# Optimization experiments

Measured on AMD Instinct MI355X. Metric: run time of the kernel, lower is better.

## Reference

```python
import jax, jax.numpy as jnp
import numpy as np

D_MODEL = 1024
N_HEADS = 16
D_HEAD = D_MODEL // N_HEADS


def setup_inputs() -> dict:
    key = jax.random.key(0)
    ks = jax.random.split(key, 5)
    B, T = 2, 2048
    x = jax.random.normal(ks[0], (B, T, D_MODEL), dtype=jnp.float32)
    s = 1.0 / np.sqrt(D_MODEL)
    W_qkv = jax.random.normal(ks[1], (D_MODEL, 3 * D_MODEL), dtype=jnp.float32) * s
    b_qkv = jnp.zeros((3 * D_MODEL,), dtype=jnp.float32)
    W_proj = jax.random.normal(ks[2], (D_MODEL, D_MODEL), dtype=jnp.float32) * s
    b_proj = jnp.zeros((D_MODEL,), dtype=jnp.float32)
    return {"x": x, "W_qkv": W_qkv, "b_qkv": b_qkv, "W_proj": W_proj, "b_proj": b_proj}


def reference(x, W_qkv, b_qkv, W_proj, b_proj):
    B, T, C = x.shape
    qkv = x @ W_qkv + b_qkv                      # [B,T,3C]
    q, k, v = jnp.split(qkv, 3, axis=-1)
    # [B,T,C] -> [B,H,T,Dh]
    def to_heads(t):
        return t.reshape(B, T, N_HEADS, D_HEAD).transpose(0, 2, 1, 3)
    q, k, v = to_heads(q), to_heads(k), to_heads(v)
    scale = 1.0 / np.sqrt(D_HEAD).astype(np.float32)
    scores = jnp.einsum('bhqd,bhkd->bhqk', q, k) * scale  # [B,H,T,T]
    causal = jnp.tril(jnp.ones((T, T), dtype=bool))
    scores = jnp.where(causal, scores, -jnp.inf)
    attn = jax.nn.softmax(scores, axis=-1)
    out = jnp.einsum('bhqk,bhkd->bhqd', attn, v)          # [B,H,T,Dh]
    out = out.transpose(0, 2, 1, 3).reshape(B, T, C)
    return out @ W_proj + b_proj
```

## Files before the change

### kernel.cpp

```cpp
#include <hip/hip_runtime.h>
#include <hip/hip_bf16.h>
#include <cstdint>


using u16 = unsigned short;
using u32 = unsigned int;

typedef __bf16 bf16x8 __attribute__((ext_vector_type(8)));
typedef float f32x4 __attribute__((ext_vector_type(4)));

#define AS1 __attribute__((address_space(1)))
#define AS3 __attribute__((address_space(3)))

__device__ __forceinline__ u16 f2bf(float f) {
  u32 u = __float_as_uint(f);
  u += 0x7fffu + ((u >> 16) & 1u);
  return (u16)(u >> 16);
}
__device__ __forceinline__ u32 pack2bf(float a, float b) {
  u32 ua = __float_as_uint(a) + 0x8000u;
  u32 ub = __float_as_uint(b) + 0x8000u;
  return (ua >> 16) | (ub & 0xffff0000u);
}

__global__ __launch_bounds__(256) void prep(const float* __restrict__ x,
                                            u16* __restrict__ xb,
                                            const float* __restrict__ W0,
                                            u16* __restrict__ T0,
                                            const float* __restrict__ W1,
                                            u16* __restrict__ T1) {
  const int bx = blockIdx.x;
  const int tid = threadIdx.x;
  if (bx < 4096) {
    const int i = bx * 256 + tid;
    float4 v = ((const float4*)x)[i];
    ushort4 o;
    o.x = f2bf(v.x); o.y = f2bf(v.y); o.z = f2bf(v.z); o.w = f2bf(v.w);
    ((ushort4*)xb)[i] = o;
    return;
  }
  __shared__ float t[32][33];
  const int idx = bx - 4096;
  const int bxx = idx & 127, by = idx >> 7;
  const float* W; u16* Wt; int N, n0;
  if (bxx < 96) { W = W0; Wt = T0; N = 3072; n0 = bxx * 32; }
  else          { W = W1; Wt = T1; N = 1024; n0 = (bxx - 96) * 32; }
  const int k0 = by * 32;
  const int tx = tid & 31, ty = tid >> 5;
#pragma unroll
  for (int i = 0; i < 4; ++i)
    t[ty + i * 8][tx] = W[(size_t)(k0 + ty + i * 8) * N + n0 + tx];
  __syncthreads();
#pragma unroll
  for (int i = 0; i < 4; ++i)
    Wt[(size_t)(n0 + ty + i * 8) * 1024 + k0 + tx] = f2bf(t[tx][ty + i * 8]);
}

#define MFMA16 __builtin_amdgcn_mfma_f32_16x16x32_bf16

__global__ __launch_bounds__(512, 2) void gemm_qkv(const u16* __restrict__ A,
                                                   const u16* __restrict__ Bt,
                                                   const float* __restrict__ bias,
                                                   u16* __restrict__ qb,
                                                   u16* __restrict__ KF,
                                                   u16* __restrict__ VF,
                                                   float sc_val) {
  constexpr int NT = 16;
  constexpr int BUFO = 7 * 4096;
  __shared__ __align__(16) u16 sm[2 * BUFO];

  const int tid  = threadIdx.x;
  const int lane = tid & 63;
  const int w    = tid >> 6;
  const int quad = lane >> 4;
  const int l15  = lane & 15;

  const int bid = blockIdx.x;
  const int xcd = bid & 7, c = bid >> 3;
  const int mt = (xcd >> 1) * 4 + (c & 3);
  const int nt = (xcd & 1) * 8 + (c >> 2);
  const int bm = mt * 256, bn = nt * 192;

  const int wr = (w >> 2) * 128;
  const int wc = (w & 3) * 48;

  const int srow = tid >> 3;
  const int scol = (((tid & 7) ^ ((tid >> 3) & 7)) << 3);

#define STAGEA(ch, ktile, bufo)                                                 \
  __builtin_amdgcn_global_load_lds(                                             \
      (AS1 const void*)(A + (size_t)(bm + (ch) * 64 + srow) * 1024 +            \
                        ((ktile) << 6) + scol),                                 \
      (AS3 void*)(sm + (bufo) + (ch) * 4096 + tid * 8), 16, 0, 0)
#define STAGEB(ch, ktile, bufo)                                                 \
  __builtin_amdgcn_global_load_lds(                                             \
      (AS1 const void*)(Bt + (size_t)(bn + (ch) * 64 + srow) * 1024 +           \
                        ((ktile) << 6) + scol),                                 \
      (AS3 void*)(sm + (bufo) + (4 + (ch)) * 4096 + tid * 8), 16, 0, 0)

  const int ca = (w >> 2) * 2;
  int abase_lo[4], abase_hi[4], bbase[3];
#pragma unroll
  for (int mi = 0; mi < 4; ++mi) {
    abase_lo[mi] = (ca + 0) * 4096 + (mi * 16 + l15) * 64;
    abase_hi[mi] = (ca + 1) * 4096 + (mi * 16 + l15) * 64;
  }
#pragma unroll
  for (int ni = 0; ni < 3; ++ni) {
    const int rb = wc + ni * 16 + l15;
    bbase[ni] = (4 + (rb >> 6)) * 4096 + (rb & 63) * 64;
  }
  const int sw0 = ((quad ^ (l15 & 7)) << 3);
  const int sw1 = sw0 ^ 32;

  STAGEA(0, 0, 0); STAGEA(1, 0, 0); STAGEA(2, 0, 0); STAGEA(3, 0, 0);
  STAGEB(0, 0, 0); STAGEB(1, 0, 0); STAGEB(2, 0, 0);
  STAGEB(0, 1, BUFO); STAGEB(1, 1, BUFO);
  STAGEB(2, 1, BUFO); STAGEA(0, 1, BUFO); STAGEA(1, 1, BUFO);
  asm volatile("s_waitcnt vmcnt(5)" ::: "memory");
  __builtin_amdgcn_s_barrier();

  f32x4 acc[8][3] = {};
  bf16x8 alo[4][2], ahi[4][2], b[3][2];

#pragma unroll 2
  for (int j = 0; j < NT; ++j) {
    const int bo  = (j & 1) * BUFO;
    const int nbo = bo ^ BUFO;
    const u16* smb = sm + bo;

#pragma unroll
    for (int mi = 0; mi < 4; ++mi) {
      alo[mi][0] = *(const bf16x8*)(smb + abase_lo[mi] + sw0);
      alo[mi][1] = *(const bf16x8*)(smb + abase_lo[mi] + sw1);
    }
#pragma unroll
    for (int ni = 0; ni < 2; ++ni) {
      b[ni][0] = *(const bf16x8*)(smb + bbase[ni] + sw0);
      b[ni][1] = *(const bf16x8*)(smb + bbase[ni] + sw1);
    }
    if (j + 1 < NT) { STAGEA(2, j + 1, nbo); STAGEA(3, j + 1, nbo); }
    __builtin_amdgcn_s_barrier();
    asm volatile("s_waitcnt lgkmcnt(0)" ::: "memory");
    __builtin_amdgcn_s_setprio(1);
#pragma unroll
    for (int mi = 0; mi < 4; ++mi)
#pragma unroll
      for (int ni = 0; ni < 2; ++ni) {
        acc[mi][ni] = MFMA16(alo[mi][0], b[ni][0], acc[mi][ni], 0, 0, 0);
        acc[mi][ni] = MFMA16(alo[mi][1], b[ni][1], acc[mi][ni], 0, 0, 0);
      }
    __builtin_amdgcn_s_setprio(0);
    __builtin_amdgcn_s_barrier();

#pragma unroll
    for (int mi = 0; mi < 4; ++mi) {
      ahi[mi][0] = *(const bf16x8*)(smb + abase_hi[mi] + sw0);
      ahi[mi][1] = *(const bf16x8*)(smb + abase_hi[mi] + sw1);
    }
    b[2][0] = *(const bf16x8*)(smb + bbase[2] + sw0);
    b[2][1] = *(const bf16x8*)(smb + bbase[2] + sw1);
    if (j + 2 < NT) { STAGEB(0, j + 2, bo); STAGEB(1, j + 2, bo); }
    __builtin_amdgcn_s_barrier();
    asm volatile("s_waitcnt lgkmcnt(0)" ::: "memory");
    __builtin_amdgcn_s_setprio(1);
#pragma unroll
    for (int mi = 0; mi < 4; ++mi) {
      acc[mi][2] = MFMA16(alo[mi][0], b[2][0], acc[mi][2], 0, 0, 0);
      acc[mi][2] = MFMA16(alo[mi][1], b[2][1], acc[mi][2], 0, 0, 0);
      acc[4 + mi][0] = MFMA16(ahi[mi][0], b[0][0], acc[4 + mi][0], 0, 0, 0);
      acc[4 + mi][0] = MFMA16(ahi[mi][1], b[0][1], acc[4 + mi][0], 0, 0, 0);
    }
    __builtin_amdgcn_s_setprio(0);
    __builtin_amdgcn_s_barrier();

    if (j + 2 < NT) { STAGEB(2, j + 2, bo); STAGEA(0, j + 2, bo); STAGEA(1, j + 2, bo); }
    __builtin_amdgcn_s_barrier();
    __builtin_amdgcn_s_setprio(1);
#pragma unroll
    for (int mi = 0; mi < 4; ++mi)
#pragma unroll
      for (int ni = 1; ni < 3; ++ni) {
        acc[4 + mi][ni] = MFMA16(ahi[mi][0], b[ni][0], acc[4 + mi][ni], 0, 0, 0);
        acc[4 + mi][ni] = MFMA16(ahi[mi][1], b[ni][1], acc[4 + mi][ni], 0, 0, 0);
      }
    __builtin_amdgcn_s_setprio(0);
    if (j + 2 < NT)
      asm volatile("s_waitcnt vmcnt(5)" ::: "memory");
    else
      asm volatile("s_waitcnt vmcnt(0)" ::: "memory");
    __builtin_amdgcn_s_barrier();
  }
#undef STAGEA
#undef STAGEB

  const int crow0 = bm + wr + (quad << 2);
  const int ccol0 = bn + wc + l15;
#pragma unroll
  for (int ni = 0; ni < 3; ++ni) {
    const int n = ccol0 + ni * 16;
    const float bv = bias[n];
    if (n < 1024) {
#pragma unroll
      for (int mi = 0; mi < 8; ++mi) {
        const int m0 = crow0 + mi * 16;
#pragma unroll
        for (int r = 0; r < 4; ++r)
          qb[(size_t)(m0 + r) * 1024 + n] = f2bf((acc[mi][ni][r] + bv) * sc_val);
      }
    } else if (n < 2048) {
      const int hk = (n - 1024) >> 6;
      const int d  = (n - 1024) & 63;
      const int hh = d >> 5, qd = (d >> 3) & 3, jj = d & 7;
#pragma unroll
      for (int mi = 0; mi < 8; ++mi) {
#pragma unroll
        for (int r = 0; r < 4; ++r) {
          const int t  = crow0 + mi * 16 + r;
          const int bb = t >> 11, tt = t & 2047;
          const int kt = tt >> 6, mm = (tt >> 4) & 3, l = tt & 15;
          KF[((size_t)((bb * 16 + hk) * 32 + kt) * 8 + mm * 2 + hh) * 512 +
             (qd * 16 + l) * 8 + jj] = f2bf(acc[mi][ni][r] + bv);
        }
      }
    } else {
      const int hv = (n - 2048) >> 6;
      const int d  = (n - 2048) & 63;
      const int di = d >> 4, l = d & 15;
#pragma unroll
      for (int mi = 0; mi < 8; ++mi) {
#pragma unroll
        for (int r = 0; r < 4; ++r) {
          const int t  = crow0 + mi * 16 + r;
          const int bb = t >> 11, tt = t & 2047;
          const int kt = tt >> 6, to = tt & 63;
          const int mq = to >> 4, qd2 = (to >> 2) & 3, rr = to & 3;
          const int hh = mq >> 1, jj = (mq & 1) * 4 + rr;
          VF[((size_t)((bb * 16 + hv) * 32 + kt) * 8 + hh * 4 + di) * 512 +
             (qd2 * 16 + l) * 8 + jj] = f2bf(acc[mi][ni][r] + bv);
        }
      }
    }
  }
}

__global__ __launch_bounds__(256) void gemm_proj(const u16* __restrict__ A,
                                                 const u16* __restrict__ Bt,
                                                 const float* __restrict__ bias,
                                                 float* __restrict__ C) {
  constexpr int BM = 128, BN = 64, BK = 32;
  constexpr int K = 1024, N = 1024;
  __shared__ __align__(16) u16 lA[BM * BK];
  __shared__ __align__(16) u16 lB[BN * BK];
  const int tid  = threadIdx.x;
  const int lane = tid & 63;
  const int wave = tid >> 6;
  const int bm = blockIdx.x * BM;
  const int bn = blockIdx.y * BN;
  const int wr = wave * 32;

  f32x4 acc[2][4] = {};

  const int f0 = (wave << 10) + (lane << 4);
  const int f1 = f0 + 4096;
  const int ar0 = f0 >> 6, ac0 = (f0 & 63) >> 1;
  const int ar1 = f1 >> 6, ac1 = (f1 & 63) >> 1;

  const int arow = wr + (lane & 15);
  const int brow = (lane & 15);
  const int kk   = (lane >> 4) << 3;

  for (int k0 = 0; k0 < K; k0 += BK) {
    __builtin_amdgcn_global_load_lds((AS1 const void*)(A + (size_t)(bm + ar0) * K + k0 + ac0),
                                     (AS3 void*)(lA + (wave << 9)), 16, 0, 0);
    __builtin_amdgcn_global_load_lds((AS1 const void*)(A + (size_t)(bm + ar1) * K + k0 + ac1),
                                     (AS3 void*)(lA + ((wave + 4) << 9)), 16, 0, 0);
    __builtin_amdgcn_global_load_lds((AS1 const void*)(Bt + (size_t)(bn + ar0) * K + k0 + ac0),
                                     (AS3 void*)(lB + (wave << 9)), 16, 0, 0);
    __syncthreads();

    bf16x8 af[2], bfr[4];
#pragma unroll
    for (int mi = 0; mi < 2; ++mi)
      af[mi] = *(const bf16x8*)&lA[(arow + mi * 16) * BK + kk];
#pragma unroll
    for (int ni = 0; ni < 4; ++ni)
      bfr[ni] = *(const bf16x8*)&lB[(brow + ni * 16) * BK + kk];
#pragma unroll
    for (int mi = 0; mi < 2; ++mi)
#pragma unroll
      for (int ni = 0; ni < 4; ++ni)
        acc[mi][ni] = __builtin_amdgcn_mfma_f32_16x16x32_bf16(af[mi], bfr[ni],
                                                              acc[mi][ni], 0, 0, 0);
    __syncthreads();
  }

  const int crow0 = bm + wr + ((lane >> 4) << 2);
  const int ccol0 = bn + (lane & 15);
#pragma unroll
  for (int ni = 0; ni < 4; ++ni) {
    const int n = ccol0 + ni * 16;
    const float bv = bias[n];
#pragma unroll
    for (int mi = 0; mi < 2; ++mi) {
      const int m0 = crow0 + mi * 16;
#pragma unroll
      for (int r = 0; r < 4; ++r)
        C[(size_t)(m0 + r) * N + n] = acc[mi][ni][r] + bv;
    }
  }
}

__global__ __launch_bounds__(256) void attn_bal(const u16* __restrict__ qb,
                                                const u16* __restrict__ KF,
                                                const u16* __restrict__ VF,
                                                u16* __restrict__ out) {
  const int f  = blockIdx.x;
  const int u  = (f >> 3) & 31;
  const int bh = (f & 7) | ((f >> 8) << 3);
  const int b = bh >> 4, h = bh & 15;
  const int tid = threadIdx.x;
  const int lane = tid & 63;
  const int w    = tid >> 6;
  const int quad = lane >> 4;
  const int l15  = lane & 15;
  const int g32 = (w & 1) ? (63 - u) : u;
  const int par = w >> 1;
  const int q0 = g32 * 32;
  const int ktmax = g32 >> 1;

  __shared__ float CB[2][64][35];

  const u16* qbase = qb + (size_t)b * 2048 * 1024 + h * 64;
  bf16x8 qf[2][2];
#pragma unroll
  for (int g = 0; g < 2; ++g)
#pragma unroll
    for (int hh = 0; hh < 2; ++hh)
      qf[g][hh] = *(const bf16x8*)(qbase + (size_t)(q0 + g * 16 + l15) * 1024 +
                                   hh * 32 + quad * 8);

  const size_t fb = (size_t)bh * 32 * 4096 + lane * 8;
  const u16* kfb = KF + fb;
  const u16* vfb = VF + fb;

  f32x4 accO[2][4] = {};
  float lrow[2] = {0.f, 0.f};

  bf16x8 kcur[4][2];
  {
    const u16* kp = kfb + (size_t)par * 4096;
#pragma unroll
    for (int m = 0; m < 4; ++m)
#pragma unroll
      for (int hh = 0; hh < 2; ++hh)
        kcur[m][hh] = *(const bf16x8*)(kp + (m * 2 + hh) * 512);
  }

  for (int kt = par; kt <= ktmax; kt += 2) {
    const u16* vp = vfb + (size_t)kt * 4096;
    bf16x8 vfr[2][4];
#pragma unroll
    for (int hh = 0; hh < 2; ++hh)
#pragma unroll
      for (int di = 0; di < 4; ++di)
        vfr[hh][di] = *(const bf16x8*)(vp + (hh * 4 + di) * 512);
    const int ktn = (kt + 2 <= ktmax) ? kt + 2 : ktmax;
    const u16* kpn = kfb + (size_t)ktn * 4096;
    bf16x8 knx[4][2];
#pragma unroll
    for (int m = 0; m < 4; ++m)
#pragma unroll
      for (int hh = 0; hh < 2; ++hh)
        knx[m][hh] = *(const bf16x8*)(kpn + (m * 2 + hh) * 512);

    const bool diag = (kt == ktmax);
    bf16x8 ap[2][2];
#pragma unroll
    for (int g = 0; g < 2; ++g) {
      f32x4 sT[4] = {};
#pragma unroll
      for (int m = 0; m < 4; ++m) {
        sT[m] = __builtin_amdgcn_mfma_f32_16x16x32_bf16(kcur[m][0], qf[g][0], sT[m], 0, 0, 0);
        sT[m] = __builtin_amdgcn_mfma_f32_16x16x32_bf16(kcur[m][1], qf[g][1], sT[m], 0, 0, 0);
      }
      float pv[4][4];
      if (diag) {
        const int qgl = q0 + g * 16 + l15;
#pragma unroll
        for (int m = 0; m < 4; ++m)
#pragma unroll
          for (int r = 0; r < 4; ++r) {
            const bool msk = (kt * 64 + m * 16 + quad * 4 + r) > qgl;
            pv[m][r] = msk ? 0.f : __builtin_amdgcn_exp2f(sT[m][r]);
          }
      } else {
#pragma unroll
        for (int m = 0; m < 4; ++m)
#pragma unroll
          for (int r = 0; r < 4; ++r)
            pv[m][r] = __builtin_amdgcn_exp2f(sT[m][r]);
      }
      const float s0 = (pv[0][0] + pv[0][1]) + (pv[0][2] + pv[0][3]);
      const float s1 = (pv[1][0] + pv[1][1]) + (pv[1][2] + pv[1][3]);
      const float s2 = (pv[2][0] + pv[2][1]) + (pv[2][2] + pv[2][3]);
      const float s3 = (pv[3][0] + pv[3][1]) + (pv[3][2] + pv[3][3]);
      lrow[g] += (s0 + s1) + (s2 + s3);

      union { u32 u4[4]; bf16x8 v; } t0, t1;
      t0.u4[0] = pack2bf(pv[0][0], pv[0][1]);
      t0.u4[1] = pack2bf(pv[0][2], pv[0][3]);
      t0.u4[2] = pack2bf(pv[1][0], pv[1][1]);
      t0.u4[3] = pack2bf(pv[1][2], pv[1][3]);
      t1.u4[0] = pack2bf(pv[2][0], pv[2][1]);
      t1.u4[1] = pack2bf(pv[2][2], pv[2][3]);
      t1.u4[2] = pack2bf(pv[3][0], pv[3][1]);
      t1.u4[3] = pack2bf(pv[3][2], pv[3][3]);
      ap[g][0] = t0.v;
      ap[g][1] = t1.v;
    }

#pragma unroll
    for (int hh = 0; hh < 2; ++hh)
#pragma unroll
      for (int di = 0; di < 4; ++di) {
        bf16x8 bv = vfr[hh][di];
#pragma unroll
        for (int g = 0; g < 2; ++g)
          accO[g][di] = __builtin_amdgcn_mfma_f32_16x16x32_bf16(ap[g][hh], bv,
                                                               accO[g][di], 0, 0, 0);
      }

#pragma unroll
    for (int m = 0; m < 4; ++m)
#pragma unroll
      for (int hh = 0; hh < 2; ++hh)
        kcur[m][hh] = knx[m][hh];
  }

  if (par) {
    float* cb = CB[w & 1][lane];
#pragma unroll
    for (int g = 0; g < 2; ++g)
#pragma unroll
      for (int di = 0; di < 4; ++di)
#pragma unroll
        for (int r = 0; r < 4; ++r)
          cb[g * 16 + di * 4 + r] = accO[g][di][r];
    cb[32] = lrow[0];
    cb[33] = lrow[1];
  }
  __syncthreads();
  if (!par) {
    const float* cb = CB[w & 1][lane];
#pragma unroll
    for (int g = 0; g < 2; ++g)
#pragma unroll
      for (int di = 0; di < 4; ++di)
#pragma unroll
        for (int r = 0; r < 4; ++r)
          accO[g][di][r] += cb[g * 16 + di * 4 + r];
    lrow[0] += cb[32];
    lrow[1] += cb[33];
#pragma unroll
    for (int g = 0; g < 2; ++g) {
      lrow[g] += __shfl_xor(lrow[g], 16);
      lrow[g] += __shfl_xor(lrow[g], 32);
    }

#pragma unroll
    for (int g = 0; g < 2; ++g)
#pragma unroll
      for (int r = 0; r < 4; ++r) {
        const float lv = __shfl(lrow[g], quad * 4 + r);
        const float inv = 1.f / lv;
        const int q = q0 + g * 16 + quad * 4 + r;
        u16* op = out + (size_t)(b * 2048 + q) * 1024 + h * 64 + l15;
#pragma unroll
        for (int di = 0; di < 4; ++di)
          op[di * 16] = f2bf(accO[g][di][r] * inv);
      }
  }
}

extern "C" void kernel_launch(void* const* d_in, const int* in_sizes, int n_in,
                              void* d_out, int out_size, void* d_ws, size_t ws_size,
                              hipStream_t stream) {
  const float* x     = (const float*)d_in[0];
  const float* Wqkv  = (const float*)d_in[1];
  const float* bqkv  = (const float*)d_in[2];
  const float* Wproj = (const float*)d_in[3];
  const float* bproj = (const float*)d_in[4];
  float* out = (float*)d_out;

  char* ws = (char*)d_ws;
  u16* xb     = (u16*)(ws);
  u16* wqkvT  = (u16*)(ws + 8388608);
  u16* wprojT = (u16*)(ws + 14680064);
  u16* qb     = (u16*)(ws + 16777216);
  u16* KF     = (u16*)(ws + 25165824);
  u16* VF     = (u16*)(ws + 33554432);
  u16* att    = (u16*)(ws + 41943040);

  constexpr float cs = 0.18033688011f;

  prep<<<8192, 256, 0, stream>>>(x, xb, Wqkv, wqkvT, Wproj, wprojT);

  gemm_qkv<<<dim3(256), 512, 0, stream>>>(xb, wqkvT, bqkv, qb, KF, VF, cs);

  attn_bal<<<dim3(1024), 256, 0, stream>>>(qb, KF, VF, att);

  gemm_proj<<<dim3(32, 16), 256, 0, stream>>>(att, wprojT, bproj, out);
}
```

Before: 168.1 us.

## Split attention blocks to one query tile each, compute row sums via MFMA

Attention blocks now hold 128 threads handling a single 32-row query tile, scheduled longest-first, in place of pairing short and long tiles inside 256-thread blocks. Row sums of probabilities come from an MFMA against a ones vector, replacing the VALU adds and shuffles. The loop is manually unrolled so K double-buffers swap without register copies, and bf16 packing uses the hardware v_cvt_pk_bf16_f32 instruction. In exchange it adds extra MFMA work for the row sums, and the converter rounds to nearest-even where the old pack rounded half up. MFMA16 is used but its definition is not visible, so it may be defined elsewhere.

```diff
diff --git a/kernel.cpp b/kernel.cpp
--- a/kernel.cpp
+++ b/kernel.cpp
@@ -17,10 +17,10 @@
   u += 0x7fffu + ((u >> 16) & 1u);
   return (u16)(u >> 16);
 }
-__device__ __forceinline__ u32 pack2bf(float a, float b) {
-  u32 ua = __float_as_uint(a) + 0x8000u;
-  u32 ub = __float_as_uint(b) + 0x8000u;
-  return (ua >> 16) | (ub & 0xffff0000u);
+__device__ __forceinline__ u32 cvtpk(float a, float b) {
+  u32 r;
+  asm("v_cvt_pk_bf16_f32 %0, %1, %2" : "=v"(r) : "v"(a), "v"(b));
+  return r;
 }
 
 __global__ __launch_bounds__(256) void prep(const float* __restrict__ x,
@@ -311,25 +311,23 @@
   }
 }
 
-__global__ __launch_bounds__(256) void attn_bal(const u16* __restrict__ qb,
+__global__ __launch_bounds__(128) void attn_bal(const u16* __restrict__ qb,
                                                 const u16* __restrict__ KF,
                                                 const u16* __restrict__ VF,
                                                 u16* __restrict__ out) {
-  const int f  = blockIdx.x;
-  const int u  = (f >> 3) & 31;
-  const int bh = (f & 7) | ((f >> 8) << 3);
+  const int bid = blockIdx.x;
+  const int g32 = 63 - ((bid >> 3) & 63);
+  const int bh  = (bid & 7) | ((bid >> 9) << 3);
   const int b = bh >> 4, h = bh & 15;
   const int tid = threadIdx.x;
   const int lane = tid & 63;
-  const int w    = tid >> 6;
+  const int par  = tid >> 6;
   const int quad = lane >> 4;
   const int l15  = lane & 15;
-  const int g32 = (w & 1) ? (63 - u) : u;
-  const int par = w >> 1;
   const int q0 = g32 * 32;
   const int ktmax = g32 >> 1;
 
-  __shared__ float CB[2][64][35];
+  __shared__ float CB[64][41];
 
   const u16* qbase = qb + (size_t)b * 2048 * 1024 + h * 64;
   bf16x8 qf[2][2];
@@ -345,19 +343,23 @@
   const u16* vfb = VF + fb;
 
   f32x4 accO[2][4] = {};
-  float lrow[2] = {0.f, 0.f};
-
-  bf16x8 kcur[4][2];
+  f32x4 accL[2] = {};
+
+  union { u32 u4[4]; bf16x8 v; } onesu;
+  onesu.u4[0] = onesu.u4[1] = onesu.u4[2] = onesu.u4[3] = 0x3f803f80u;
+  const bf16x8 onesf = onesu.v;
+
+  bf16x8 kA[4][2], kB[4][2];
   {
     const u16* kp = kfb + (size_t)par * 4096;
 #pragma unroll
     for (int m = 0; m < 4; ++m)
 #pragma unroll
       for (int hh = 0; hh < 2; ++hh)
-        kcur[m][hh] = *(const bf16x8*)(kp + (m * 2 + hh) * 512);
-  }
-
-  for (int kt = par; kt <= ktmax; kt += 2) {
+        kA[m][hh] = *(const bf16x8*)(kp + (m * 2 + hh) * 512);
+  }
+
+  auto tile = [&](int kt, bf16x8 (&KC)[4][2], bf16x8 (&KN)[4][2]) {
     const u16* vp = vfb + (size_t)kt * 4096;
     bf16x8 vfr[2][4];
 #pragma unroll
@@ -367,12 +369,11 @@
         vfr[hh][di] = *(const bf16x8*)(vp + (hh * 4 + di) * 512);
     const int ktn = (kt + 2 <= ktmax) ? kt + 2 : ktmax;
     const u16* kpn = kfb + (size_t)ktn * 4096;
-    bf16x8 knx[4][2];
 #pragma unroll
     for (int m = 0; m < 4; ++m)
 #pragma unroll
       for (int hh = 0; hh < 2; ++hh)
-        knx[m][hh] = *(const bf16x8*)(kpn + (m * 2 + hh) * 512);
+        KN[m][hh] = *(const bf16x8*)(kpn + (m * 2 + hh) * 512);
 
     const bool diag = (kt == ktmax);
     bf16x8 ap[2][2];
@@ -381,8 +382,8 @@
       f32x4 sT[4] = {};
 #pragma unroll
       for (int m = 0; m < 4; ++m) {
-        sT[m] = __builtin_amdgcn_mfma_f32_16x16x32_bf16(kcur[m][0], qf[g][0], sT[m], 0, 0, 0);
-        sT[m] = __builtin_amdgcn_mfma_f32_16x16x32_bf16(kcur[m][1], qf[g][1], sT[m], 0, 0, 0);
+        sT[m] = MFMA16(KC[m][0], qf[g][0], sT[m], 0, 0, 0);
+        sT[m] = MFMA16(KC[m][1], qf[g][1], sT[m], 0, 0, 0);
       }
       float pv[4][4];
       if (diag) {
@@ -401,21 +402,15 @@
           for (int r = 0; r < 4; ++r)
             pv[m][r] = __builtin_amdgcn_exp2f(sT[m][r]);
       }
-      const float s0 = (pv[0][0] + pv[0][1]) + (pv[0][2] + pv[0][3]);
-      const float s1 = (pv[1][0] + pv[1][1]) + (pv[1][2] + pv[1][3]);
-      const float s2 = (pv[2][0] + pv[2][1]) + (pv[2][2] + pv[2][3]);
-      const float s3 = (pv[3][0] + pv[3][1]) + (pv[3][2] + pv[3][3]);
-      lrow[g] += (s0 + s1) + (s2 + s3);
-
       union { u32 u4[4]; bf16x8 v; } t0, t1;
-      t0.u4[0] = pack2bf(pv[0][0], pv[0][1]);
-      t0.u4[1] = pack2bf(pv[0][2], pv[0][3]);
-      t0.u4[2] = pack2bf(pv[1][0], pv[1][1]);
-      t0.u4[3] = pack2bf(pv[1][2], pv[1][3]);
-      t1.u4[0] = pack2bf(pv[2][0], pv[2][1]);
-      t1.u4[1] = pack2bf(pv[2][2], pv[2][3]);
-      t1.u4[2] = pack2bf(pv[3][0], pv[3][1]);
-      t1.u4[3] = pack2bf(pv[3][2], pv[3][3]);
+      t0.u4[0] = cvtpk(pv[0][0], pv[0][1]);
+      t0.u4[1] = cvtpk(pv[0][2], pv[0][3]);
+      t0.u4[2] = cvtpk(pv[1][0], pv[1][1]);
+      t0.u4[3] = cvtpk(pv[1][2], pv[1][3]);
+      t1.u4[0] = cvtpk(pv[2][0], pv[2][1]);
+      t1.u4[1] = cvtpk(pv[2][2], pv[2][3]);
+      t1.u4[2] = cvtpk(pv[3][0], pv[3][1]);
+      t1.u4[3] = cvtpk(pv[3][2], pv[3][3]);
       ap[g][0] = t0.v;
       ap[g][1] = t1.v;
     }
@@ -427,53 +422,55 @@
         bf16x8 bv = vfr[hh][di];
 #pragma unroll
         for (int g = 0; g < 2; ++g)
-          accO[g][di] = __builtin_amdgcn_mfma_f32_16x16x32_bf16(ap[g][hh], bv,
-                                                               accO[g][di], 0, 0, 0);
-      }
-
-#pragma unroll
-    for (int m = 0; m < 4; ++m)
-#pragma unroll
-      for (int hh = 0; hh < 2; ++hh)
-        kcur[m][hh] = knx[m][hh];
+          accO[g][di] = MFMA16(ap[g][hh], bv, accO[g][di], 0, 0, 0);
+      }
+#pragma unroll
+    for (int g = 0; g < 2; ++g) {
+      accL[g] = MFMA16(ap[g][0], onesf, accL[g], 0, 0, 0);
+      accL[g] = MFMA16(ap[g][1], onesf, accL[g], 0, 0, 0);
+    }
+  };
+
+  for (int kt = par; kt <= ktmax; ) {
+    tile(kt, kA, kB); kt += 2;
+    if (kt > ktmax) break;
+    tile(kt, kB, kA); kt += 2;
   }
 
   if (par) {
-    float* cb = CB[w & 1][lane];
-#pragma unroll
-    for (int g = 0; g < 2; ++g)
+    float* cb = CB[lane];
+#pragma unroll
+    for (int g = 0; g < 2; ++g) {
 #pragma unroll
       for (int di = 0; di < 4; ++di)
 #pragma unroll
         for (int r = 0; r < 4; ++r)
           cb[g * 16 + di * 4 + r] = accO[g][di][r];
-    cb[32] = lrow[0];
-    cb[33] = lrow[1];
+#pragma unroll
+      for (int r = 0; r < 4; ++r)
+        cb[32 + g * 4 + r] = accL[g][r];
+    }
   }
   __syncthreads();
   if (!par) {
-    const float* cb = CB[w & 1][lane];
-#pragma unroll
-    for (int g = 0; g < 2; ++g)
+    const float* cb = CB[lane];
+#pragma unroll
+    for (int g = 0; g < 2; ++g) {
 #pragma unroll
       for (int di = 0; di < 4; ++di)
 #pragma unroll
         for (int r = 0; r < 4; ++r)
           accO[g][di][r] += cb[g * 16 + di * 4 + r];
-    lrow[0] += cb[32];
-    lrow[1] += cb[33];
-#pragma unroll
-    for (int g = 0; g < 2; ++g) {
-      lrow[g] += __shfl_xor(lrow[g], 16);
-      lrow[g] += __shfl_xor(lrow[g], 32);
+#pragma unroll
+      for (int r = 0; r < 4; ++r)
+        accL[g][r] += cb[32 + g * 4 + r];
     }
 
 #pragma unroll
     for (int g = 0; g < 2; ++g)
 #pragma unroll
       for (int r = 0; r < 4; ++r) {
-        const float lv = __shfl(lrow[g], quad * 4 + r);
-        const float inv = 1.f / lv;
+        const float inv = 1.f / accL[g][r];
         const int q = q0 + g * 16 + quad * 4 + r;
         u16* op = out + (size_t)(b * 2048 + q) * 1024 + h * 64 + l15;
 #pragma unroll
@@ -508,7 +505,7 @@
 
   gemm_qkv<<<dim3(256), 512, 0, stream>>>(xb, wqkvT, bqkv, qb, KF, VF, cs);
 
-  attn_bal<<<dim3(1024), 256, 0, stream>>>(qb, KF, VF, att);
+  attn_bal<<<dim3(2048), 128, 0, stream>>>(qb, KF, VF, att);
 
   gemm_proj<<<dim3(32, 16), 256, 0, stream>>>(att, wprojT, bproj, out);
 }
```

Measured after the change: 168.3 us. About the same (+0.1%).
